# Optimization experiments

Measured on AMD Instinct MI355X. Metric: run time of the kernel, lower is better.

## Reference

```python
import jax, jax.numpy as jnp
import numpy as np

N_HEAD, D_MODEL, D_HEAD = 16, 1024, 64
QLEN, MLEN, BATCH = 1024, 1024, 4
KLEN = QLEN + MLEN
LN_EPS = 1e-5


def _rel_shift(x):
    # x: [q, r, b, n] -> Transformer-XL relative shift
    q, r = x.shape[0], x.shape[1]
    zero_pad = jnp.zeros((q, 1) + x.shape[2:], x.dtype)
    x_padded = jnp.concatenate([zero_pad, x], axis=1)  # [q, r+1, b, n]
    x_padded = x_padded.reshape((r + 1, q) + x.shape[2:])
    return x_padded[1:].reshape(x.shape)


def _layer_norm(x, gamma, beta):
    mu = jnp.mean(x, axis=-1, keepdims=True)
    var = jnp.var(x, axis=-1, keepdims=True)
    return (x - mu) * jax.lax.rsqrt(var + LN_EPS) * gamma + beta


def setup_inputs() -> dict:
    key = jax.random.key(0)
    ks = jax.random.split(key, 10)
    d, n, dh = D_MODEL, N_HEAD, D_HEAD
    content = jax.random.normal(ks[0], (QLEN, BATCH, d), jnp.float32)
    mems = jax.random.normal(ks[1], (MLEN, BATCH, d), jnp.float32)
    rel_pos = jax.random.normal(ks[2], (KLEN, d), jnp.float32)
    r_w_bias = jax.random.normal(ks[3], (n, dh), jnp.float32) * 0.02
    r_r_bias = jax.random.normal(ks[4], (n, dh), jnp.float32) * 0.02
    s = 1.0 / np.sqrt(d)
    W_qkv = jax.random.normal(ks[5], (d, 3 * n * dh), jnp.float32) * s
    W_r = jax.random.normal(ks[6], (d, n * dh), jnp.float32) * s
    W_o = jax.random.normal(ks[7], (n * dh, d), jnp.float32) * s
    ln_gamma = jnp.ones((d,), jnp.float32)
    ln_beta = jnp.zeros((d,), jnp.float32)
    # causal mask with memory: query i attends to keys j <= i + MLEN (True = masked)
    attn_mask = jnp.arange(KLEN)[None, :] > (jnp.arange(QLEN)[:, None] + MLEN)
    return {
        "content": content, "rel_pos": rel_pos, "mems": mems,
        "r_w_bias": r_w_bias, "r_r_bias": r_r_bias,
        "W_qkv": W_qkv, "W_r": W_r, "W_o": W_o,
        "ln_gamma": ln_gamma, "ln_beta": ln_beta,
        "attn_mask": attn_mask,
    }


def reference(content, rel_pos, mems, r_w_bias, r_r_bias, W_qkv, W_r, W_o, ln_gamma, ln_beta, attn_mask):
    qlen, b = content.shape[0], content.shape[1]
    n, dh = N_HEAD, D_HEAD
    scale = 1.0 / np.sqrt(dh)

    cat = jnp.concatenate([mems, content], axis=0)            # [klen, b, d]
    klen = cat.shape[0]
    w_heads = cat @ W_qkv                                     # [klen, b, 3*n*dh]
    w_q, w_k, w_v = jnp.split(w_heads, 3, axis=-1)
    w_q = w_q[-qlen:].reshape(qlen, b, n, dh)
    w_k = w_k.reshape(klen, b, n, dh)
    w_v = w_v.reshape(klen, b, n, dh)
    r_k = (rel_pos @ W_r).reshape(-1, n, dh)                  # [rlen, n, dh]

    AC = jnp.einsum('ibnd,jbnd->ijbn', w_q + r_w_bias, w_k)
    BD = _rel_shift(jnp.einsum('ibnd,jnd->ijbn', w_q + r_r_bias, r_k))
    attn_score = (AC + BD) * scale                            # [q, k, b, n]
    attn_score = jnp.where(attn_mask[:, :, None, None], -jnp.inf, attn_score)
    attn_prob = jax.nn.softmax(attn_score, axis=1)

    attn_vec = jnp.einsum('ijbn,jbnd->ibnd', attn_prob, w_v)
    attn_vec = attn_vec.reshape(qlen, b, n * dh)
    attn_out = attn_vec @ W_o                                 # [q, b, d]
    return _layer_norm(content + attn_out, ln_gamma, ln_beta)
```

## Files before the change

### kernel.cpp

```cpp
#include <hip/hip_runtime.h>

#define QLEN 1024
#define MLEN 1024
#define KLEN 2048
#define BATCH 4
#define NHEAD 16
#define DHEAD 64
#define DMODEL 1024

typedef _Float16 half8 __attribute__((ext_vector_type(8)));
typedef _Float16 half4 __attribute__((ext_vector_type(4)));
typedef float f32x4 __attribute__((ext_vector_type(4)));

#define NEG_INF (-__builtin_inff())
#define QSCALE 0.18033688011112042f

typedef __attribute__((address_space(3))) unsigned int lds_u32;
typedef __attribute__((address_space(1))) unsigned int glb_u32;

__device__ __forceinline__ void gll16(void* lds, const void* g) {
  __builtin_amdgcn_global_load_lds((const glb_u32*)g, (lds_u32*)lds, 16, 0, 0);
}

__global__ __launch_bounds__(256) void k_prep(const float* __restrict__ Wqkv,
                                              const float* __restrict__ Wr,
                                              const float* __restrict__ Wo,
                                              const float* __restrict__ rel_pos,
                                              const float* __restrict__ mems,
                                              const float* __restrict__ content,
                                              _Float16* __restrict__ WqkvT,
                                              _Float16* __restrict__ WrT,
                                              _Float16* __restrict__ WoT,
                                              _Float16* __restrict__ RelP,
                                              _Float16* __restrict__ Acat)
{
  __shared__ float T[64][65];
  const int z = blockIdx.z;
  const int tid = threadIdx.x;
  if (z == 3) {
    int nb = gridDim.x * gridDim.y;
    int bid = blockIdx.y * gridDim.x + blockIdx.x;
    for (int e = (bid * 256 + tid) * 4; e < KLEN * DMODEL; e += nb * 256 * 4) {
      float4 v = *(const float4*)(rel_pos + e);
      half4 o = { (_Float16)v.x, (_Float16)v.y, (_Float16)v.z, (_Float16)v.w };
      *(half4*)(RelP + e) = o;
    }
    return;
  }
  if (z == 4) {
    int nb = gridDim.x * gridDim.y;
    int bid = blockIdx.y * gridDim.x + blockIdx.x;
    for (int e = (bid * 256 + tid) * 4; e < 8192 * DMODEL; e += nb * 256 * 4) {
      int m = e >> 10, kk = e & 1023;
      int crow = m >> 2, bb = m & 3;
      const float* src;
      if (crow < MLEN) src = mems + (size_t)(crow * BATCH + bb) * DMODEL + kk;
      else             src = content + (size_t)((crow - MLEN) * BATCH + bb) * DMODEL + kk;
      float4 v = *(const float4*)src;
      half4 o = { (_Float16)v.x, (_Float16)v.y, (_Float16)v.z, (_Float16)v.w };
      *(half4*)(Acat + (size_t)m * DMODEL + kk) = o;
    }
    return;
  }
  const float* in; _Float16* out; int C;
  if (z == 0)      { in = Wqkv; out = WqkvT; C = 3072; }
  else if (z == 1) { if (blockIdx.x >= 16) return; in = Wr; out = WrT; C = 1024; }
  else             { if (blockIdx.x >= 16) return; in = Wo; out = WoT; C = 1024; }
  const int R = 1024;
  int c0 = blockIdx.x * 64, r0 = blockIdx.y * 64;
#pragma unroll
  for (int u = 0; u < 16; ++u) {
    int lin = u * 256 + tid;
    int rr = lin >> 6, cc = lin & 63;
    T[rr][cc] = in[(size_t)(r0 + rr) * C + c0 + cc];
  }
  __syncthreads();
#pragma unroll
  for (int u = 0; u < 16; ++u) {
    int lin = u * 256 + tid;
    int cc = lin >> 6, rr = lin & 63;
    out[(size_t)(c0 + cc) * R + r0 + rr] = (_Float16)T[rr][cc];
  }
}

__global__ __launch_bounds__(256) void k_trans_v(const _Float16* __restrict__ Vb,
                                                 _Float16* __restrict__ VbT)
{
  __shared__ _Float16 T[64][72];
  int r0 = blockIdx.x * 64;
  int bh = blockIdx.y;
  const _Float16* in = Vb + (size_t)bh * KLEN * DHEAD;
  _Float16* out = VbT + (size_t)bh * DHEAD * KLEN;
  int tid = threadIdx.x;
#pragma unroll
  for (int u = 0; u < 16; ++u) {
    int lin = u * 256 + tid;
    int rr = lin >> 6, cc = lin & 63;
    T[rr][cc] = in[(size_t)(r0 + rr) * DHEAD + cc];
  }
  __syncthreads();
#pragma unroll
  for (int u = 0; u < 16; ++u) {
    int lin = u * 256 + tid;
    int cc = lin >> 6, rr = lin & 63;
    out[(size_t)cc * KLEN + r0 + rr] = T[rr][cc];
  }
}

template<typename Epi>
__device__ __forceinline__ void gemm_tile_128(const _Float16* __restrict__ A,
                                              const _Float16* __restrict__ B,
                                              int K, int m0, int n0,
                                              _Float16* As, _Float16* Bs, Epi epi)
{
  const int tid = threadIdx.x;
  const int lane = tid & 63;
  const int wave = tid >> 6;
  const int q = lane >> 4, l16 = lane & 15;
  const int wm = wave >> 1, wn = wave & 1;
  f32x4 acc[4][4] = {};

  for (int k0 = 0; k0 < K; k0 += 32) {
    __syncthreads();
#pragma unroll
    for (int i = 0; i < 2; ++i) {
      int c = i * 256 + tid;
      int row = c >> 2, pos = c & 3;
      int col8 = pos ^ ((row >> 1) & 3);
      gll16(&As[c * 8], A + (size_t)(m0 + row) * K + k0 + col8 * 8);
      gll16(&Bs[c * 8], B + (size_t)(n0 + row) * K + k0 + col8 * 8);
    }
    __syncthreads();
    half8 a[4], b[4];
#pragma unroll
    for (int rt = 0; rt < 4; ++rt) {
      int row = wm * 64 + rt * 16 + l16;
      a[rt] = *(const half8*)&As[(row * 4 + (q ^ ((row >> 1) & 3))) * 8];
    }
#pragma unroll
    for (int ct = 0; ct < 4; ++ct) {
      int row = wn * 64 + ct * 16 + l16;
      b[ct] = *(const half8*)&Bs[(row * 4 + (q ^ ((row >> 1) & 3))) * 8];
    }
#pragma unroll
    for (int rt = 0; rt < 4; ++rt)
#pragma unroll
      for (int ct = 0; ct < 4; ++ct)
        acc[rt][ct] = __builtin_amdgcn_mfma_f32_16x16x32_f16(a[rt], b[ct], acc[rt][ct], 0, 0, 0);
  }
#pragma unroll
  for (int rt = 0; rt < 4; ++rt)
#pragma unroll
    for (int ct = 0; ct < 4; ++ct)
#pragma unroll
      for (int reg = 0; reg < 4; ++reg) {
        int m = m0 + wm * 64 + rt * 16 + q * 4 + reg;
        int nn = n0 + wn * 64 + ct * 16 + l16;
        epi(m, nn, acc[rt][ct][reg]);
      }
}

__global__ __launch_bounds__(256, 2) void k_gemm_qkv_rk(
    const _Float16* __restrict__ A, const _Float16* __restrict__ B,
    const _Float16* __restrict__ RelP, const _Float16* __restrict__ WrT,
    _Float16* __restrict__ Qw, _Float16* __restrict__ Qr,
    _Float16* __restrict__ Kb, _Float16* __restrict__ Vb,
    _Float16* __restrict__ Rk2,
    const float* __restrict__ rwb, const float* __restrict__ rrb)
{
  __shared__ __align__(16) _Float16 As[128 * 32];
  __shared__ __align__(16) _Float16 Bs[128 * 32];
  const int bx = blockIdx.x, by = blockIdx.y;
  if (by >= 64) {
    if (bx >= 8) return;
    gemm_tile_128(RelP, WrT, DMODEL, (by - 64) * 128, bx * 128, As, Bs,
      [=](int m, int nn, float v) {
        int hh = nn >> 6, dd = nn & 63;
        Rk2[((size_t)hh * KLEN + m) * DHEAD + dd] = (_Float16)v;
      });
    return;
  }
  if (bx < 8 && by < 32) return;
  const int sec = bx >> 3;
  gemm_tile_128(A, B, DMODEL, by * 128, bx * 128, As, Bs,
    [=](int m, int nn, float v) {
      int c = nn & 1023;
      int hh = c >> 6, dd = c & 63;
      int crow = m >> 2, bb = m & 3;
      int bhh = bb * NHEAD + hh;
      if (sec == 0) {
        int i = crow - MLEN;
        size_t o = ((size_t)bhh * QLEN + i) * DHEAD + dd;
        Qw[o] = (_Float16)((v + rwb[c]) * QSCALE);
        Qr[o] = (_Float16)((v + rrb[c]) * QSCALE);
      } else if (sec == 1) {
        Kb[((size_t)bhh * KLEN + crow) * DHEAD + dd] = (_Float16)v;
      } else {
        Vb[((size_t)bhh * KLEN + crow) * DHEAD + dd] = (_Float16)v;
      }
    });
}

__global__ __launch_bounds__(256, 2) void k_gemm_out(
    const _Float16* __restrict__ A, const _Float16* __restrict__ B,
    const float* __restrict__ content, float* __restrict__ Y)
{
  __shared__ __align__(16) _Float16 As[128 * 32];
  __shared__ __align__(16) _Float16 Bs[128 * 32];
  gemm_tile_128(A, B, DMODEL, blockIdx.y * 128, blockIdx.x * 128, As, Bs,
    [=](int m, int nn, float v) {
      Y[(size_t)m * DMODEL + nn] = v + content[(size_t)m * DMODEL + nn];
    });
}

__global__ __launch_bounds__(256, 2) void k_attn(
    const _Float16* __restrict__ Qw, const _Float16* __restrict__ Qr,
    const _Float16* __restrict__ Kb, const _Float16* __restrict__ VbT,
    const _Float16* __restrict__ Rk2, _Float16* __restrict__ AV)
{
  __shared__ __align__(16) _Float16 Kl[2][64 * 64];
  __shared__ __align__(16) _Float16 Vtl[2][64 * 64];
  __shared__ __align__(16) _Float16 Pl[4][16 * 64];

  const int tid = threadIdx.x;
  const int lane = tid & 63, wave = tid >> 6;
  const int q = lane >> 4, l16 = lane & 15;
  const int bh = blockIdx.x & 63;
  const int xq = blockIdx.x >> 6;
  const int i0 = (15 - xq) * 64;
  const int h = bh & 15, bb = bh >> 4;

  const _Float16* Qwb = Qw + (size_t)bh * QLEN * DHEAD;
  const _Float16* Qrb = Qr + (size_t)bh * QLEN * DHEAD;
  const _Float16* Kbb = Kb + (size_t)bh * KLEN * DHEAD;
  const _Float16* Vtb = VbT + (size_t)bh * DHEAD * KLEN;
  const _Float16* Rkb = Rk2 + (size_t)h * KLEN * DHEAD;

  const int iw = i0 + wave * 16;
  const int lim = iw + 15 + MLEN;

  half8 aqw[2], aqr[2];
#pragma unroll
  for (int s = 0; s < 2; ++s) {
    size_t o = (size_t)(iw + l16) * DHEAD + s * 32 + q * 8;
    aqw[s] = *(const half8*)(Qwb + o);
    aqr[s] = *(const half8*)(Qrb + o);
  }

  f32x4 oa[4] = {};
  float l_lane[4] = {};
  _Float16* Plw = &Pl[wave][0];

  auto stageK = [&](int j0s, int bufi) {
#pragma unroll
    for (int i = 0; i < 2; ++i) {
      int c = i * 256 + tid;
      int row = c >> 3;
      int col8 = (c & 7) ^ (row & 7);
      gll16(&Kl[bufi][c * 8], Kbb + (size_t)(j0s + row) * DHEAD + col8 * 8);
    }
  };
  auto stageV = [&](int j0s, int bufi) {
#pragma unroll
    for (int i = 0; i < 2; ++i) {
      int c = i * 256 + tid;
      int row = c >> 3;
      int col8 = (c & 7) ^ (row & 7);
      gll16(&Vtl[bufi][c * 8], Vtb + (size_t)row * KLEN + j0s + col8 * 8);
    }
  };
  auto loadRK = [&](int j0t, half8 (&rk)[5][2]) {
    const int rs = j0t - iw + 1008;
#pragma unroll
    for (int rt = 0; rt < 5; ++rt) {
      int r = rs + rt * 16 + l16;
      int rc = r < 0 ? 0 : (r > KLEN - 1 ? KLEN - 1 : r);
      const _Float16* base = Rkb + (size_t)rc * DHEAD + q * 8;
      rk[rt][0] = *(const half8*)(base);
      rk[rt][1] = *(const half8*)(base + 32);
    }
  };
  auto computeAC = [&](const _Float16* Klb, f32x4 (&ac)[4]) {
#pragma unroll
    for (int ct = 0; ct < 4; ++ct) {
      int row = ct * 16 + l16;
#pragma unroll
      for (int s = 0; s < 2; ++s) {
        int pos = (s * 4 + q) ^ (row & 7);
        half8 bk = *(const half8*)&Klb[(row * 8 + pos) * 8];
        ac[ct] = __builtin_amdgcn_mfma_f32_16x16x32_f16(aqw[s], bk, ac[ct], 0, 0, 0);
      }
    }
  };
  auto computeBD = [&](half8 (&rk)[5][2], f32x4 (&bd)[5]) {
#pragma unroll
    for (int rt = 0; rt < 5; ++rt) {
      bd[rt] = __builtin_amdgcn_mfma_f32_16x16x32_f16(aqr[0], rk[rt][0], bd[rt], 0, 0, 0);
      bd[rt] = __builtin_amdgcn_mfma_f32_16x16x32_f16(aqr[1], rk[rt][1], bd[rt], 0, 0, 0);
    }
  };

  const int n_jt = (i0 >> 6) + 17;

  stageK(0, 0);
  stageV(0, 0);
  __syncthreads();
  stageK(64, 1);
  f32x4 ac_p[4] = {}, bd_p[5] = {};
  {
    half8 rk0[5][2];
    loadRK(0, rk0);
    computeAC(Kl[0], ac_p);
    computeBD(rk0, bd_p);
  }

  for (int jt = 0; jt < n_jt; ++jt) {
    const int j0 = jt * 64;
    __syncthreads();
    if (jt + 2 < n_jt) stageK((jt + 2) * 64, jt & 1);
    if (jt + 1 < n_jt) stageV((jt + 1) * 64, (jt + 1) & 1);

    const bool act  = (j0 <= lim);
    const bool actn = (j0 + 64 <= lim) && (jt + 1 < n_jt);

    f32x4 ac_n[4] = {};
    if (actn) computeAC(Kl[(jt + 1) & 1], ac_n);

    if (act) {
      const bool boundary = (j0 + 63 > iw + MLEN);
#pragma unroll
      for (int reg = 0; reg < 4; ++reg) {
        const int m = q * 4 + reg;
        const int src = (l16 + 15 - m) & 15;
        float sh[5];
#pragma unroll
        for (int rt = 0; rt < 5; ++rt) sh[rt] = __shfl(bd_p[rt][reg], src, 16);
        const bool sel = (l16 > m);
        float acc = 0.f;
        if (!boundary) {
#pragma unroll
          for (int ct = 0; ct < 4; ++ct) {
            float bdv = sel ? sh[ct + 1] : sh[ct];
            float e = __builtin_amdgcn_exp2f(ac_p[ct][reg] + bdv);
            acc += e;
            int c = ct * 16 + l16;
            Plw[m * 64 + (((c >> 3) ^ (m & 7)) * 8) + (c & 7)] = (_Float16)e;
          }
        } else {
#pragma unroll
          for (int ct = 0; ct < 4; ++ct) {
            float bdv = sel ? sh[ct + 1] : sh[ct];
            float sv = ac_p[ct][reg] + bdv;
            if (j0 + ct * 16 + l16 > iw + m + MLEN) sv = NEG_INF;
            float e = __builtin_amdgcn_exp2f(sv);
            acc += e;
            int c = ct * 16 + l16;
            Plw[m * 64 + (((c >> 3) ^ (m & 7)) * 8) + (c & 7)] = (_Float16)e;
          }
        }
        l_lane[reg] += acc;
      }
    }

    half8 rk[5][2];
    if (actn) loadRK((jt + 1) * 64, rk);

    if (act) {
      half8 ap[2];
#pragma unroll
      for (int s = 0; s < 2; ++s)
        ap[s] = *(const half8*)&Plw[l16 * 64 + (((s * 4 + q) ^ (l16 & 7)) * 8)];
      const _Float16* Vtlb = Vtl[jt & 1];
#pragma unroll
      for (int t = 0; t < 4; ++t) {
        int row = t * 16 + l16;
#pragma unroll
        for (int s = 0; s < 2; ++s) {
          int pos = (s * 4 + q) ^ (row & 7);
          half8 bv = *(const half8*)&Vtlb[(row * 8 + pos) * 8];
          oa[t] = __builtin_amdgcn_mfma_f32_16x16x32_f16(ap[s], bv, oa[t], 0, 0, 0);
        }
      }
    }

    if (actn) {
#pragma unroll
      for (int rt = 0; rt < 5; ++rt) bd_p[rt] = f32x4{0.f, 0.f, 0.f, 0.f};
      computeBD(rk, bd_p);
    }
#pragma unroll
    for (int ct = 0; ct < 4; ++ct) ac_p[ct] = ac_n[ct];
  }

  float linv[4];
#pragma unroll
  for (int reg = 0; reg < 4; ++reg) {
    float v = l_lane[reg];
    v += __shfl_xor(v, 1, 16);
    v += __shfl_xor(v, 2, 16);
    v += __shfl_xor(v, 4, 16);
    v += __shfl_xor(v, 8, 16);
    linv[reg] = 1.0f / v;
  }
#pragma unroll
  for (int t = 0; t < 4; ++t)
#pragma unroll
    for (int reg = 0; reg < 4; ++reg) {
      int ii = iw + q * 4 + reg;
      AV[(size_t)(ii * BATCH + bb) * DMODEL + h * DHEAD + t * 16 + l16] =
          (_Float16)(oa[t][reg] * linv[reg]);
    }
}

__global__ __launch_bounds__(256) void k_ln(const float* __restrict__ Y,
                                            const float* __restrict__ gamma,
                                            const float* __restrict__ beta,
                                            float* __restrict__ out)
{
  int row = blockIdx.x, tid = threadIdx.x;
  const float4 v = ((const float4*)(Y + (size_t)row * DMODEL))[tid];
  float s = v.x + v.y + v.z + v.w;
  float ss = v.x * v.x + v.y * v.y + v.z * v.z + v.w * v.w;
#pragma unroll
  for (int off = 32; off >= 1; off >>= 1) {
    s += __shfl_xor(s, off, 64);
    ss += __shfl_xor(ss, off, 64);
  }
  __shared__ float red[8];
  int wave = tid >> 6, lane = tid & 63;
  if (lane == 0) { red[wave] = s; red[4 + wave] = ss; }
  __syncthreads();
  s = red[0] + red[1] + red[2] + red[3];
  ss = red[4] + red[5] + red[6] + red[7];
  float mu = s * (1.0f / DMODEL);
  float var = ss * (1.0f / DMODEL) - mu * mu;
  float rstd = rsqrtf(var + 1e-5f);
  const float4 g = ((const float4*)gamma)[tid];
  const float4 bt = ((const float4*)beta)[tid];
  float4 o;
  o.x = (v.x - mu) * rstd * g.x + bt.x;
  o.y = (v.y - mu) * rstd * g.y + bt.y;
  o.z = (v.z - mu) * rstd * g.z + bt.z;
  o.w = (v.w - mu) * rstd * g.w + bt.w;
  ((float4*)(out + (size_t)row * DMODEL))[tid] = o;
}

extern "C" void kernel_launch(void* const* d_in, const int* in_sizes, int n_in,
                              void* d_out, int out_size, void* d_ws, size_t ws_size,
                              hipStream_t stream)
{
  (void)in_sizes; (void)n_in; (void)out_size; (void)ws_size;
  const float* content = (const float*)d_in[0];
  const float* rel_pos = (const float*)d_in[1];
  const float* mems    = (const float*)d_in[2];
  const float* rwb     = (const float*)d_in[3];
  const float* rrb     = (const float*)d_in[4];
  const float* Wqkv    = (const float*)d_in[5];
  const float* Wr      = (const float*)d_in[6];
  const float* Wo      = (const float*)d_in[7];
  const float* gamma   = (const float*)d_in[8];
  const float* beta    = (const float*)d_in[9];

  char* ws = (char*)d_ws;
  size_t off = 0;
  auto take = [&](size_t bytes) { char* p = ws + off; off += (bytes + 255) & ~(size_t)255; return p; };

  _Float16* Acat  = (_Float16*)take(8192ull * 1024 * 2);
  _Float16* WqkvT = (_Float16*)take(3072ull * 1024 * 2);
  _Float16* RelP  = (_Float16*)take(2048ull * 1024 * 2);
  _Float16* WrT   = (_Float16*)take(1024ull * 1024 * 2);
  _Float16* WoT   = (_Float16*)take(1024ull * 1024 * 2);
  _Float16* Qw    = (_Float16*)take(64ull * 1024 * 64 * 2);
  _Float16* Qr    = (_Float16*)take(64ull * 1024 * 64 * 2);
  _Float16* Kb    = (_Float16*)take(64ull * 2048 * 64 * 2);
  _Float16* Vb    = (_Float16*)take(64ull * 2048 * 64 * 2);
  _Float16* AV    = (_Float16*)take(4096ull * 1024 * 2);
  _Float16* Rk2   = (_Float16*)take(16ull * 2048 * 64 * 2);
  _Float16* VbT   = Acat;
  float*    Y     = (float*)Kb;
  float*    out   = (float*)d_out;

  k_prep<<<dim3(48, 16, 5), dim3(256), 0, stream>>>(Wqkv, Wr, Wo, rel_pos, mems, content,
                                                    WqkvT, WrT, WoT, RelP, Acat);
  k_gemm_qkv_rk<<<dim3(24, 80), dim3(256), 0, stream>>>(Acat, WqkvT, RelP, WrT,
                                                        Qw, Qr, Kb, Vb, Rk2, rwb, rrb);
  k_trans_v<<<dim3(32, 64), dim3(256), 0, stream>>>(Vb, VbT);
  k_attn<<<dim3(1024), dim3(256), 0, stream>>>(Qw, Qr, Kb, VbT, Rk2, AV);
  k_gemm_out<<<dim3(8, 32), dim3(256), 0, stream>>>(AV, WoT, content, Y);
  k_ln<<<dim3(4096), dim3(256), 0, stream>>>(Y, gamma, beta, out);
}
```

Before: 395.2 us.

## Split attention key loop into chunks with separate combine kernel

Splits each attention block's key-tile loop into chunks of 8 tiles and launches four times as many blocks. Each chunk writes unnormalized partial outputs and row sums, and a new combine kernel adds them and normalizes. This works because no running max is kept, so partial exp sums add directly. The aim is better load balance and occupancy for the causal workload, at the cost of extra global writes and reads for the partials, an extra launch, and some early-exiting blocks. The loop also issues the RK loads and next-tile staging earlier to overlap with compute.

```diff
diff --git a/kernel.cpp b/kernel.cpp
--- a/kernel.cpp
+++ b/kernel.cpp
@@ -213,10 +213,13 @@
     });
 }
 
+#define CHTILES 8
+
 __global__ __launch_bounds__(256, 2) void k_attn(
     const _Float16* __restrict__ Qw, const _Float16* __restrict__ Qr,
     const _Float16* __restrict__ Kb, const _Float16* __restrict__ VbT,
-    const _Float16* __restrict__ Rk2, _Float16* __restrict__ AV)
+    const _Float16* __restrict__ Rk2, _Float16* __restrict__ AVp,
+    float* __restrict__ lp)
 {
   __shared__ __align__(16) _Float16 Kl[2][64 * 64];
   __shared__ __align__(16) _Float16 Vtl[2][64 * 64];
@@ -226,8 +229,13 @@
   const int lane = tid & 63, wave = tid >> 6;
   const int q = lane >> 4, l16 = lane & 15;
   const int bh = blockIdx.x & 63;
-  const int xq = blockIdx.x >> 6;
-  const int i0 = (15 - xq) * 64;
+  const int xq = (blockIdx.x >> 6) & 15;
+  const int ch = blockIdx.x >> 10;
+  const int n_jt_blk = xq + 17;
+  const int jt0 = ch * CHTILES;
+  const int jtend = min(jt0 + CHTILES, n_jt_blk);
+  if (jt0 >= jtend) return;
+  const int i0 = xq * 64;
   const int h = bh & 15, bb = bh >> 4;
 
   const _Float16* Qwb = Qw + (size_t)bh * QLEN * DHEAD;
@@ -251,26 +259,26 @@
   float l_lane[4] = {};
   _Float16* Plw = &Pl[wave][0];
 
-  auto stageK = [&](int j0s, int bufi) {
+  auto stageK = [&](int jt_s) {
 #pragma unroll
     for (int i = 0; i < 2; ++i) {
       int c = i * 256 + tid;
       int row = c >> 3;
       int col8 = (c & 7) ^ (row & 7);
-      gll16(&Kl[bufi][c * 8], Kbb + (size_t)(j0s + row) * DHEAD + col8 * 8);
+      gll16(&Kl[jt_s & 1][c * 8], Kbb + (size_t)(jt_s * 64 + row) * DHEAD + col8 * 8);
     }
   };
-  auto stageV = [&](int j0s, int bufi) {
+  auto stageV = [&](int jt_s) {
 #pragma unroll
     for (int i = 0; i < 2; ++i) {
       int c = i * 256 + tid;
       int row = c >> 3;
       int col8 = (c & 7) ^ (row & 7);
-      gll16(&Vtl[bufi][c * 8], Vtb + (size_t)row * KLEN + j0s + col8 * 8);
+      gll16(&Vtl[jt_s & 1][c * 8], Vtb + (size_t)row * KLEN + jt_s * 64 + col8 * 8);
     }
   };
-  auto loadRK = [&](int j0t, half8 (&rk)[5][2]) {
-    const int rs = j0t - iw + 1008;
+  auto loadRK = [&](int jt_t, half8 (&rk)[5][2]) {
+    const int rs = jt_t * 64 - iw + 1008;
 #pragma unroll
     for (int rt = 0; rt < 5; ++rt) {
       int r = rs + rt * 16 + l16;
@@ -300,28 +308,29 @@
     }
   };
 
-  const int n_jt = (i0 >> 6) + 17;
-
-  stageK(0, 0);
-  stageV(0, 0);
+  stageK(jt0);
+  stageV(jt0);
   __syncthreads();
-  stageK(64, 1);
+  if (jt0 + 1 < jtend) stageK(jt0 + 1);
   f32x4 ac_p[4] = {}, bd_p[5] = {};
-  {
+  if (jt0 * 64 <= lim) {
     half8 rk0[5][2];
-    loadRK(0, rk0);
-    computeAC(Kl[0], ac_p);
+    loadRK(jt0, rk0);
+    computeAC(Kl[jt0 & 1], ac_p);
     computeBD(rk0, bd_p);
   }
 
-  for (int jt = 0; jt < n_jt; ++jt) {
+  for (int jt = jt0; jt < jtend; ++jt) {
     const int j0 = jt * 64;
     __syncthreads();
-    if (jt + 2 < n_jt) stageK((jt + 2) * 64, jt & 1);
-    if (jt + 1 < n_jt) stageV((jt + 1) * 64, (jt + 1) & 1);
 
     const bool act  = (j0 <= lim);
-    const bool actn = (j0 + 64 <= lim) && (jt + 1 < n_jt);
+    const bool actn = (jt + 1 < jtend) && (j0 + 64 <= lim);
+
+    half8 rk[5][2];
+    if (actn) loadRK(jt + 1, rk);
+    if (jt + 2 < jtend) stageK(jt + 2);
+    if (jt + 1 < jtend) stageV(jt + 1);
 
     f32x4 ac_n[4] = {};
     if (actn) computeAC(Kl[(jt + 1) & 1], ac_n);
@@ -360,12 +369,7 @@
         }
         l_lane[reg] += acc;
       }
-    }
-
-    half8 rk[5][2];
-    if (actn) loadRK((jt + 1) * 64, rk);
-
-    if (act) {
+
       half8 ap[2];
 #pragma unroll
       for (int s = 0; s < 2; ++s)
@@ -392,7 +396,7 @@
     for (int ct = 0; ct < 4; ++ct) ac_p[ct] = ac_n[ct];
   }
 
-  float linv[4];
+  float l_red[4];
 #pragma unroll
   for (int reg = 0; reg < 4; ++reg) {
     float v = l_lane[reg];
@@ -400,16 +404,45 @@
     v += __shfl_xor(v, 2, 16);
     v += __shfl_xor(v, 4, 16);
     v += __shfl_xor(v, 8, 16);
-    linv[reg] = 1.0f / v;
-  }
+    l_red[reg] = v;
+  }
+  _Float16* AVpc = AVp + (size_t)ch * 4096 * DMODEL;
 #pragma unroll
   for (int t = 0; t < 4; ++t)
 #pragma unroll
     for (int reg = 0; reg < 4; ++reg) {
       int ii = iw + q * 4 + reg;
-      AV[(size_t)(ii * BATCH + bb) * DMODEL + h * DHEAD + t * 16 + l16] =
-          (_Float16)(oa[t][reg] * linv[reg]);
-    }
+      AVpc[(size_t)(ii * BATCH + bb) * DMODEL + h * DHEAD + t * 16 + l16] =
+          (_Float16)oa[t][reg];
+    }
+  if (l16 == 0) {
+#pragma unroll
+    for (int reg = 0; reg < 4; ++reg)
+      lp[((size_t)ch * 64 + bh) * QLEN + iw + q * 4 + reg] = l_red[reg];
+  }
+}
+
+__global__ __launch_bounds__(256) void k_combine(const _Float16* __restrict__ AVp,
+                                                 const float* __restrict__ lp,
+                                                 _Float16* __restrict__ AV)
+{
+  const int row = blockIdx.x;
+  const int i = row >> 2, bb = row & 3;
+  const int nch = ((i >> 6) + 24) >> 3;
+  const int col = threadIdx.x * 4;
+  const int h = col >> 6;
+  const int bh = bb * NHEAD + h;
+  float l = 0.f;
+  for (int c = 0; c < nch; ++c) l += lp[((size_t)c * 64 + bh) * QLEN + i];
+  const float inv = 1.0f / l;
+  float o0 = 0.f, o1 = 0.f, o2 = 0.f, o3 = 0.f;
+  for (int c = 0; c < nch; ++c) {
+    half4 p = *(const half4*)(AVp + ((size_t)c * 4096 + row) * DMODEL + col);
+    o0 += (float)p[0]; o1 += (float)p[1]; o2 += (float)p[2]; o3 += (float)p[3];
+  }
+  half4 r = { (_Float16)(o0 * inv), (_Float16)(o1 * inv),
+              (_Float16)(o2 * inv), (_Float16)(o3 * inv) };
+  *(half4*)(AV + (size_t)row * DMODEL + col) = r;
 }
 
 __global__ __launch_bounds__(256) void k_ln(const float* __restrict__ Y,
@@ -476,6 +509,8 @@
   _Float16* Vb    = (_Float16*)take(64ull * 2048 * 64 * 2);
   _Float16* AV    = (_Float16*)take(4096ull * 1024 * 2);
   _Float16* Rk2   = (_Float16*)take(16ull * 2048 * 64 * 2);
+  _Float16* AVp   = (_Float16*)take(4ull * 4096 * 1024 * 2);
+  float*    lp    = (float*)take(4ull * 64 * 1024 * 4);
   _Float16* VbT   = Acat;
   float*    Y     = (float*)Kb;
   float*    out   = (float*)d_out;
@@ -485,7 +520,8 @@
   k_gemm_qkv_rk<<<dim3(24, 80), dim3(256), 0, stream>>>(Acat, WqkvT, RelP, WrT,
                                                         Qw, Qr, Kb, Vb, Rk2, rwb, rrb);
   k_trans_v<<<dim3(32, 64), dim3(256), 0, stream>>>(Vb, VbT);
-  k_attn<<<dim3(1024), dim3(256), 0, stream>>>(Qw, Qr, Kb, VbT, Rk2, AV);
+  k_attn<<<dim3(4096), dim3(256), 0, stream>>>(Qw, Qr, Kb, VbT, Rk2, AVp, lp);
+  k_combine<<<dim3(4096), dim3(256), 0, stream>>>(AVp, lp, AV);
   k_gemm_out<<<dim3(8, 32), dim3(256), 0, stream>>>(AV, WoT, content, Y);
   k_ln<<<dim3(4096), dim3(256), 0, stream>>>(Y, gamma, beta, out);
 }
```

Result: slower. 417.6 us (+5.7%).
